# Performance work log

Hardware: AMD Instinct MI355X
Metric: run time of the kernel (lower is better)

Reference implementation:

```python
import jax, jax.numpy as jnp
import numpy as np

N_NODES = 100000
N_EDGES = 1600000
IN_CH, EDGE_DIM, HIDDEN, OUT_CH = 3, 3, 64, 1


def setup_inputs() -> dict:
    key = jax.random.key(0)
    ks = jax.random.split(key, 10)
    x = jax.random.normal(ks[0], (N_NODES, IN_CH), dtype=jnp.float32)
    edge_index = jax.random.randint(ks[1], (2, N_EDGES), 0, N_NODES, dtype=jnp.int64)
    edge_attr = jax.random.normal(ks[2], (N_EDGES, EDGE_DIM), dtype=jnp.float32)
    # Linear params (torch Linear: y = x @ W.T + b); we store W as (in, out)
    s1 = 1.0 / np.sqrt(IN_CH + EDGE_DIM)
    W1 = jax.random.uniform(ks[3], (IN_CH + EDGE_DIM, HIDDEN), jnp.float32, -s1, s1)
    b1 = jax.random.uniform(ks[4], (HIDDEN,), jnp.float32, -s1, s1)
    s2 = 1.0 / np.sqrt(HIDDEN + EDGE_DIM)
    W2 = jax.random.uniform(ks[5], (HIDDEN + EDGE_DIM, HIDDEN), jnp.float32, -s2, s2)
    b2 = jax.random.uniform(ks[6], (HIDDEN,), jnp.float32, -s2, s2)
    s3 = 1.0 / np.sqrt(HIDDEN)
    W3 = jax.random.uniform(ks[7], (HIDDEN, OUT_CH), jnp.float32, -s3, s3)
    b3 = jax.random.uniform(ks[8], (OUT_CH,), jnp.float32, -s3, s3)
    return {"x": x, "edge_index": edge_index, "edge_attr": edge_attr,
            "W1": W1, "b1": b1, "W2": W2, "b2": b2, "W3": W3, "b3": b3}


def _edge_conv(h, src, dst, edge_attr, W, b, n_nodes):
    # gather source node features, concat edge_attr, linear, scatter-add at dst
    msg = jnp.concatenate([h[src], edge_attr], axis=-1) @ W + b  # [E, out]
    return jax.ops.segment_sum(msg, dst, num_segments=n_nodes)   # [N, out]


def reference(x, edge_index, edge_attr, W1, b1, W2, b2, W3, b3):
    src, dst = edge_index[0], edge_index[1]  # PyG source_to_target: aggregate at edge_index[1]
    n = x.shape[0]
    h = jax.nn.relu(_edge_conv(x, src, dst, edge_attr, W1, b1, n))
    h = jax.nn.relu(_edge_conv(h, src, dst, edge_attr, W2, b2, n))
    return h @ W3 + b3  # (n_nodes, 1) anomaly logits
```

## Files before the change

### kernel.cpp

```cpp
#include <hip/hip_runtime.h>

#define N_NODES 100000
#define N_EDGES 1600000
#define NCHUNK 512
#define CHUNK_E (N_EDGES / NCHUNK)
#define BSHIFT 6
#define BMASK 63
#define NBUCK 1563
#define CAP 16
#define CSRB 1536
#define REC_CAP 1536


typedef unsigned int uint4_ev __attribute__((ext_vector_type(4)));
typedef short bf16x8 __attribute__((ext_vector_type(8)));
typedef float f32x4 __attribute__((ext_vector_type(4)));

__device__ __forceinline__ unsigned short f2bf(float f) {
    unsigned int u = __float_as_uint(f);
    unsigned int r = (u + 0x7fff + ((u >> 16) & 1)) >> 16;
    return (unsigned short)r;
}
__device__ __forceinline__ unsigned int pack2bf(float a, float b) {
    return (unsigned int)f2bf(a) | ((unsigned int)f2bf(b) << 16);
}
__device__ __forceinline__ float bflo(unsigned int v) { return __uint_as_float(v << 16); }
__device__ __forceinline__ float bfhi(unsigned int v) { return __uint_as_float(v & 0xffff0000u); }

__device__ __forceinline__ float4 nt_load4(const float4* p) {
    uint4_ev v = __builtin_nontemporal_load((const uint4_ev*)p);
    return make_float4(__uint_as_float(v.x), __uint_as_float(v.y),
                       __uint_as_float(v.z), __uint_as_float(v.w));
}

__device__ __forceinline__ int wave_incl_scan(int v, int lane) {
#pragma unroll
    for (int off = 1; off < 64; off <<= 1) {
        int t = __shfl_up(v, off, 64);
        if (lane >= off) v += t;
    }
    return v;
}

__global__ __launch_bounds__(1024) void k_scatter(const int* __restrict__ ei,
                                                  const float* __restrict__ ea,
                                                  const float* __restrict__ W2,
                                                  unsigned short* __restrict__ wpk,
                                                  const float* __restrict__ x,
                                                  float4* __restrict__ xp,
                                                  int* __restrict__ cnt,
                                                  float4* __restrict__ stg) {
    const int g = blockIdx.x, t = threadIdx.x;
    if (g > NCHUNK) {
        int i = (g - NCHUNK - 1) * 1024 + t;
        if (i < N_NODES)
            xp[i] = make_float4(x[i * 3 + 0], x[i * 3 + 1], x[i * 3 + 2], 0.f);
        return;
    }
    if (g == NCHUNK) {
        if (t < 512) {
            int lane = t & 63, hh = (t >> 6) & 1, nt = t >> 7;
            int col = nt * 16 + (lane & 15);
            int k0 = hh * 32 + (lane >> 4) * 8;
#pragma unroll
            for (int j = 0; j < 8; j++)
                wpk[t * 8 + j] = f2bf(W2[(k0 + j) * 64 + col]);
        }
        return;
    }
    __shared__ int cur[NBUCK];
    for (int i = t; i < NBUCK; i += 1024) cur[i] = 0;
    __syncthreads();
    const int base = g * CHUNK_E;
    for (int i = t; i < CHUNK_E; i += 1024) {
        int e = base + i;
        int src = ei[e];
        int dst = ei[N_EDGES + e];
        float a0 = ea[(size_t)e * 3 + 0];
        float a1 = ea[(size_t)e * 3 + 1];
        float a2 = ea[(size_t)e * 3 + 2];
        int b = dst >> BSHIFT;
        int p = atomicAdd(&cur[b], 1);
        if (p < CAP) {
            unsigned pk = (unsigned)src | ((unsigned)(dst & BMASK) << 17);
            stg[((size_t)g * NBUCK + b) * CAP + p] =
                make_float4(__uint_as_float(pk), a0, a1, a2);
        }
    }
    __syncthreads();
    for (int i = t; i < NBUCK; i += 1024) cnt[g * NBUCK + i] = cur[i];
}

__global__ __launch_bounds__(256) void k_finalize(
    const float4* __restrict__ stg, const int* __restrict__ cnt,
    const float4* __restrict__ xp, const float* __restrict__ W1,
    const float* __restrict__ b1, const float* __restrict__ W2,
    const float* __restrict__ b2, const bf16x8* __restrict__ wpk,
    int* __restrict__ csr, int* __restrict__ rowinfo,
    unsigned int* __restrict__ zu, unsigned int* __restrict__ eu) {
    __shared__ float4 rec[REC_CAP];
    __shared__ int sbase[513];
    __shared__ int hist[64], lofs[64], curq[64];
    __shared__ float sU[64 * 3], sT[64 * 3];
    __shared__ int ws4[4];
    const int b = blockIdx.x, t = threadIdx.x;
    const int lane = t & 63, w = t >> 6;
    int c0 = min(cnt[(size_t)(2 * t) * NBUCK + b], CAP);
    int c1 = min(cnt[(size_t)(2 * t + 1) * NBUCK + b], CAP);
    int s = c0 + c1;
    int inc = wave_incl_scan(s, lane);
    if (lane == 63) ws4[w] = inc;
    __syncthreads();
    int wo = 0;
    for (int k = 0; k < w; k++) wo += ws4[k];
    int ex = wo + inc - s;
    sbase[2 * t] = ex;
    sbase[2 * t + 1] = ex + c0;
    if (t == 255) sbase[512] = ex + s;
    if (t < 64) hist[t] = 0;
    __syncthreads();
    const int cntb = sbase[512];
    float4 r_[6];
#pragma unroll
    for (int k = 0; k < 6; k++) {
        int i = t + k * 256;
        if (i < cntb) {
            int lo = 0, hi = 512;
#pragma unroll
            for (int it = 0; it < 9; it++) {
                int mid = (lo + hi) >> 1;
                if (sbase[mid] <= i) lo = mid; else hi = mid;
            }
            r_[k] = nt_load4(&stg[((size_t)lo * NBUCK + b) * CAP + (i - sbase[lo])]);
        }
    }
#pragma unroll
    for (int k = 0; k < 6; k++) {
        int i = t + k * 256;
        if (i < cntb) atomicAdd(&hist[__float_as_uint(r_[k].x) >> 17], 1);
    }
    __syncthreads();
    if (t < 64) {
        int v = hist[t];
        int in2 = wave_incl_scan(v, t);
        lofs[t] = in2 - v;
        curq[t] = in2 - v;
    }
    __syncthreads();
#pragma unroll
    for (int k = 0; k < 6; k++) {
        int i = t + k * 256;
        if (i < cntb) {
            int p = atomicAdd(&curq[__float_as_uint(r_[k].x) >> 17], 1);
            if (p < REC_CAP) rec[p] = r_[k];
        }
    }
    __syncthreads();
    {
        const int l = t >> 2, sub = t & 3;
        const int n = b * 64 + l;
        const int d = hist[l], lo = lofs[l];
        float u0 = 0, u1 = 0, u2 = 0, t0 = 0, t1 = 0, t2 = 0;
        for (int j = sub; j < d; j += 4) {
            float4 r = rec[lo + j];
            unsigned pk = __float_as_uint(r.x);
            int src = pk & 0x1FFFF;
            csr[b * CSRB + lo + j] = src;
            t0 += r.y; t1 += r.z; t2 += r.w;
            float4 xv = xp[src];
            u0 += xv.x; u1 += xv.y; u2 += xv.z;
        }
#pragma unroll
        for (int off = 1; off <= 2; off <<= 1) {
            u0 += __shfl_xor(u0, off, 64); u1 += __shfl_xor(u1, off, 64);
            u2 += __shfl_xor(u2, off, 64); t0 += __shfl_xor(t0, off, 64);
            t1 += __shfl_xor(t1, off, 64); t2 += __shfl_xor(t2, off, 64);
        }
        if (sub == 0) {
            sU[l * 3 + 0] = u0; sU[l * 3 + 1] = u1; sU[l * 3 + 2] = u2;
            sT[l * 3 + 0] = t0; sT[l * 3 + 1] = t1; sT[l * 3 + 2] = t2;
            if (n < N_NODES)
                rowinfo[n] = (int)(((unsigned)(b * CSRB + lo) << 8) | (unsigned)d);
        }
    }
    __syncthreads();
    const int tb = b * 64 + w * 16;
    if (tb >= N_NODES) return;
    const int col = lane & 15;
    const int q = lane >> 4;
    const int ln = w * 16 + col;
    const float d = (float)hist[ln];
    const float u0 = sU[ln * 3], u1 = sU[ln * 3 + 1], u2 = sU[ln * 3 + 2];
    const float t0 = sT[ln * 3], t1 = sT[ln * 3 + 1], t2 = sT[ln * 3 + 2];
    bf16x8 af[2];
#pragma unroll
    for (int h = 0; h < 2; h++) {
#pragma unroll
        for (int j = 0; j < 8; j++) {
            int c = h * 32 + q * 8 + j;
            float a = d * b1[c];
            a = fmaf(u0, W1[0 * 64 + c], a);
            a = fmaf(u1, W1[1 * 64 + c], a);
            a = fmaf(u2, W1[2 * 64 + c], a);
            a = fmaf(t0, W1[3 * 64 + c], a);
            a = fmaf(t1, W1[4 * 64 + c], a);
            a = fmaf(t2, W1[5 * 64 + c], a);
            af[h][j] = (short)f2bf(fmaxf(a, 0.f));
        }
    }
    f32x4 acc[4];
#pragma unroll
    for (int nt = 0; nt < 4; nt++) {
        bf16x8 b0 = wpk[(nt * 2 + 0) * 64 + lane];
        bf16x8 b1f = wpk[(nt * 2 + 1) * 64 + lane];
        f32x4 a = {0.f, 0.f, 0.f, 0.f};
        a = __builtin_amdgcn_mfma_f32_16x16x32_bf16(af[0], b0, a, 0, 0, 0);
        a = __builtin_amdgcn_mfma_f32_16x16x32_bf16(af[1], b1f, a, 0, 0, 0);
        acc[nt] = a;
    }
#pragma unroll
    for (int nt = 0; nt < 4; nt++) {
#pragma unroll
        for (int r = 0; r < 4; r++) {
            float v = acc[nt][r];
            float pv = __shfl_xor(v, 1, 64);
            if ((lane & 1) == 0) {
                int nr = tb + q * 4 + r;
                zu[(size_t)nr * 32 + nt * 8 + (col >> 1)] = pack2bf(v, pv);
            }
        }
    }
    const float eb = b2[lane];
    const float w64 = W2[64 * 64 + lane];
    const float w65 = W2[65 * 64 + lane];
    const float w66 = W2[66 * 64 + lane];
#pragma unroll 4
    for (int mm = 0; mm < 16; mm++) {
        int lm = w * 16 + mm;
        float dd = (float)hist[lm];
        float s0 = sT[lm * 3], s1 = sT[lm * 3 + 1], s2 = sT[lm * 3 + 2];
        float e = dd * eb;
        e = fmaf(s0, w64, e); e = fmaf(s1, w65, e); e = fmaf(s2, w66, e);
        float pe = __shfl_xor(e, 1, 64);
        if ((lane & 1) == 0)
            eu[(size_t)(tb + mm) * 32 + (lane >> 1)] = pack2bf(e, pe);
    }
}

__global__ __launch_bounds__(256) void k_agg(
    const unsigned int* __restrict__ zu, const unsigned int* __restrict__ eu,
    const int* __restrict__ rowinfo, const int* __restrict__ csr,
    const float* __restrict__ W3, const float* __restrict__ b3,
    float* __restrict__ out) {
    const int lane = threadIdx.x & 63;
    const int li = lane & 15;
    const int q = li & 7;
    const int r = li >> 3;
    const int n = blockIdx.x * 16 + (threadIdx.x >> 4);

    float cw3[8];
#pragma unroll
    for (int m = 0; m < 8; m++) cw3[m] = W3[8 * q + m];
    const float b3v = b3[0];

    const unsigned ri = (unsigned)rowinfo[n];
    const int start = (int)(ri >> 8), end = start + (int)(ri & 255u);
    float S[8];
#pragma unroll
    for (int m = 0; m < 8; m++) S[m] = 0.f;

    for (int c = start; c < end; c += 16) {
        int idx[8];
        float mk[8];
        uint4 v[8];
#pragma unroll
        for (int u = 0; u < 8; u++) {
            int i = c + 2 * u + r;
            bool ok = i < end;
            mk[u] = ok ? 1.f : 0.f;
            idx[u] = csr[ok ? i : start];
        }
#pragma unroll
        for (int u = 0; u < 8; u++)
            v[u] = *(const uint4*)&zu[(size_t)idx[u] * 32 + q * 4];
#pragma unroll
        for (int u = 0; u < 8; u++) {
            S[0] = fmaf(mk[u], bflo(v[u].x), S[0]); S[1] = fmaf(mk[u], bfhi(v[u].x), S[1]);
            S[2] = fmaf(mk[u], bflo(v[u].y), S[2]); S[3] = fmaf(mk[u], bfhi(v[u].y), S[3]);
            S[4] = fmaf(mk[u], bflo(v[u].z), S[4]); S[5] = fmaf(mk[u], bfhi(v[u].z), S[5]);
            S[6] = fmaf(mk[u], bflo(v[u].w), S[6]); S[7] = fmaf(mk[u], bfhi(v[u].w), S[7]);
        }
    }
#pragma unroll
    for (int m = 0; m < 8; m++) S[m] += __shfl_xor(S[m], 8, 64);

    const uint4 ev = *(const uint4*)&eu[(size_t)n * 32 + q * 4];
    float contrib;
    {
        float h0 = fmaxf(S[0] + bflo(ev.x), 0.f);
        float h1v = fmaxf(S[1] + bfhi(ev.x), 0.f);
        float h2v = fmaxf(S[2] + bflo(ev.y), 0.f);
        float h3 = fmaxf(S[3] + bfhi(ev.y), 0.f);
        float h4 = fmaxf(S[4] + bflo(ev.z), 0.f);
        float h5 = fmaxf(S[5] + bfhi(ev.z), 0.f);
        float h6 = fmaxf(S[6] + bflo(ev.w), 0.f);
        float h7 = fmaxf(S[7] + bfhi(ev.w), 0.f);
        contrib = h0 * cw3[0];
        contrib = fmaf(h1v, cw3[1], contrib);
        contrib = fmaf(h2v, cw3[2], contrib);
        contrib = fmaf(h3, cw3[3], contrib);
        contrib = fmaf(h4, cw3[4], contrib);
        contrib = fmaf(h5, cw3[5], contrib);
        contrib = fmaf(h6, cw3[6], contrib);
        contrib = fmaf(h7, cw3[7], contrib);
    }
    contrib += __shfl_xor(contrib, 1, 64);
    contrib += __shfl_xor(contrib, 2, 64);
    contrib += __shfl_xor(contrib, 4, 64);
    if (li == 0) out[n] = contrib + b3v;
}

extern "C" void kernel_launch(void* const* d_in, const int* in_sizes, int n_in,
                              void* d_out, int out_size, void* d_ws, size_t ws_size,
                              hipStream_t stream) {
    const float* x  = (const float*)d_in[0];
    const int*   ei = (const int*)d_in[1];
    const float* ea = (const float*)d_in[2];
    const float* W1 = (const float*)d_in[3];
    const float* b1 = (const float*)d_in[4];
    const float* W2 = (const float*)d_in[5];
    const float* b2 = (const float*)d_in[6];
    const float* W3 = (const float*)d_in[7];
    const float* b3 = (const float*)d_in[8];
    float* out = (float*)d_out;

    char* ws = (char*)d_ws;
    int*    cnt     = (int*)(ws + 0);
    int*    rowinfo = (int*)(ws + 3201024);
    int*    csr     = (int*)(ws + 3601152);
    unsigned int* zu = (unsigned int*)(ws + 13204224);
    unsigned int* eu = (unsigned int*)(ws + 26004224);
    unsigned short* wpk = (unsigned short*)(ws + 38804224);
    float4* xp  = (float4*)(ws + 38812416);
    float4* stg = (float4*)(ws + 40412416);

    k_scatter<<<NCHUNK + 99, 1024, 0, stream>>>(ei, ea, W2, wpk, x, xp, cnt, stg);
    k_finalize<<<NBUCK, 256, 0, stream>>>(stg, cnt, xp, W1, b1, W2, b2,
                                          (const bf16x8*)wpk, csr, rowinfo, zu, eu);
    k_agg<<<N_NODES / 16, 256, 0, stream>>>(zu, eu, rowinfo, csr, W3, b3, out);
}
```

Before: 183.3 us.

## Use byte counts and one-thread-per-chunk gathering in finalize with 512 threads

```diff
diff --git a/kernel.cpp b/kernel.cpp
--- a/kernel.cpp
+++ b/kernel.cpp
@@ -9,7 +9,7 @@
 #define NBUCK 1563
 #define CAP 16
 #define CSRB 1536
-#define REC_CAP 1536
+#define REC_CAP 1280
 
 
 typedef unsigned int uint4_ev __attribute__((ext_vector_type(4)));
@@ -48,7 +48,7 @@
                                                   unsigned short* __restrict__ wpk,
                                                   const float* __restrict__ x,
                                                   float4* __restrict__ xp,
-                                                  int* __restrict__ cnt,
+                                                  unsigned char* __restrict__ cnt8,
                                                   float4* __restrict__ stg) {
     const int g = blockIdx.x, t = threadIdx.x;
     if (g > NCHUNK) {
@@ -88,80 +88,49 @@
         }
     }
     __syncthreads();
-    for (int i = t; i < NBUCK; i += 1024) cnt[g * NBUCK + i] = cur[i];
-}
-
-__global__ __launch_bounds__(256) void k_finalize(
-    const float4* __restrict__ stg, const int* __restrict__ cnt,
+    for (int i = t; i < NBUCK; i += 1024)
+        cnt8[(size_t)g * NBUCK + i] = (unsigned char)min(cur[i], 255);
+}
+
+__global__ __launch_bounds__(512) void k_finalize(
+    const float4* __restrict__ stg, const unsigned char* __restrict__ cnt8,
     const float4* __restrict__ xp, const float* __restrict__ W1,
     const float* __restrict__ b1, const float* __restrict__ W2,
     const float* __restrict__ b2, const bf16x8* __restrict__ wpk,
     int* __restrict__ csr, int* __restrict__ rowinfo,
     unsigned int* __restrict__ zu, unsigned int* __restrict__ eu) {
     __shared__ float4 rec[REC_CAP];
-    __shared__ int sbase[513];
     __shared__ int hist[64], lofs[64], curq[64];
     __shared__ float sU[64 * 3], sT[64 * 3];
-    __shared__ int ws4[4];
     const int b = blockIdx.x, t = threadIdx.x;
     const int lane = t & 63, w = t >> 6;
-    int c0 = min(cnt[(size_t)(2 * t) * NBUCK + b], CAP);
-    int c1 = min(cnt[(size_t)(2 * t + 1) * NBUCK + b], CAP);
-    int s = c0 + c1;
-    int inc = wave_incl_scan(s, lane);
-    if (lane == 63) ws4[w] = inc;
-    __syncthreads();
-    int wo = 0;
-    for (int k = 0; k < w; k++) wo += ws4[k];
-    int ex = wo + inc - s;
-    sbase[2 * t] = ex;
-    sbase[2 * t + 1] = ex + c0;
-    if (t == 255) sbase[512] = ex + s;
+    const int cc = min((int)cnt8[(size_t)t * NBUCK + b], CAP);
+    const size_t sb = ((size_t)t * NBUCK + b) * CAP;
     if (t < 64) hist[t] = 0;
     __syncthreads();
-    const int cntb = sbase[512];
-    float4 r_[6];
-#pragma unroll
-    for (int k = 0; k < 6; k++) {
-        int i = t + k * 256;
-        if (i < cntb) {
-            int lo = 0, hi = 512;
-#pragma unroll
-            for (int it = 0; it < 9; it++) {
-                int mid = (lo + hi) >> 1;
-                if (sbase[mid] <= i) lo = mid; else hi = mid;
-            }
-            r_[k] = nt_load4(&stg[((size_t)lo * NBUCK + b) * CAP + (i - sbase[lo])]);
-        }
-    }
-#pragma unroll
-    for (int k = 0; k < 6; k++) {
-        int i = t + k * 256;
-        if (i < cntb) atomicAdd(&hist[__float_as_uint(r_[k].x) >> 17], 1);
-    }
+    const float* stgf = (const float*)stg;
+    for (int j = 0; j < cc; ++j)
+        atomicAdd(&hist[__float_as_uint(stgf[(sb + j) * 4]) >> 17], 1);
     __syncthreads();
     if (t < 64) {
         int v = hist[t];
-        int in2 = wave_incl_scan(v, t);
-        lofs[t] = in2 - v;
-        curq[t] = in2 - v;
-    }
-    __syncthreads();
-#pragma unroll
-    for (int k = 0; k < 6; k++) {
-        int i = t + k * 256;
-        if (i < cntb) {
-            int p = atomicAdd(&curq[__float_as_uint(r_[k].x) >> 17], 1);
-            if (p < REC_CAP) rec[p] = r_[k];
-        }
+        int inc = wave_incl_scan(v, t);
+        lofs[t] = inc - v;
+        curq[t] = inc - v;
+    }
+    __syncthreads();
+    for (int j = 0; j < cc; ++j) {
+        float4 r = nt_load4(&stg[sb + j]);
+        int p = atomicAdd(&curq[__float_as_uint(r.x) >> 17], 1);
+        if (p < REC_CAP) rec[p] = r;
     }
     __syncthreads();
     {
-        const int l = t >> 2, sub = t & 3;
+        const int l = t >> 3, sub = t & 7;
         const int n = b * 64 + l;
         const int d = hist[l], lo = lofs[l];
         float u0 = 0, u1 = 0, u2 = 0, t0 = 0, t1 = 0, t2 = 0;
-        for (int j = sub; j < d; j += 4) {
+        for (int j = sub; j < d; j += 8) {
             float4 r = rec[lo + j];
             unsigned pk = __float_as_uint(r.x);
             int src = pk & 0x1FFFF;
@@ -171,7 +140,7 @@
             u0 += xv.x; u1 += xv.y; u2 += xv.z;
         }
 #pragma unroll
-        for (int off = 1; off <= 2; off <<= 1) {
+        for (int off = 1; off <= 4; off <<= 1) {
             u0 += __shfl_xor(u0, off, 64); u1 += __shfl_xor(u1, off, 64);
             u2 += __shfl_xor(u2, off, 64); t0 += __shfl_xor(t0, off, 64);
             t1 += __shfl_xor(t1, off, 64); t2 += __shfl_xor(t2, off, 64);
@@ -184,6 +153,7 @@
         }
     }
     __syncthreads();
+    if (w >= 4) return;
     const int tb = b * 64 + w * 16;
     if (tb >= N_NODES) return;
     const int col = lane & 15;
@@ -335,17 +305,17 @@
     float* out = (float*)d_out;
 
     char* ws = (char*)d_ws;
-    int*    cnt     = (int*)(ws + 0);
-    int*    rowinfo = (int*)(ws + 3201024);
-    int*    csr     = (int*)(ws + 3601152);
-    unsigned int* zu = (unsigned int*)(ws + 13204224);
-    unsigned int* eu = (unsigned int*)(ws + 26004224);
-    unsigned short* wpk = (unsigned short*)(ws + 38804224);
-    float4* xp  = (float4*)(ws + 38812416);
-    float4* stg = (float4*)(ws + 40412416);
-
-    k_scatter<<<NCHUNK + 99, 1024, 0, stream>>>(ei, ea, W2, wpk, x, xp, cnt, stg);
-    k_finalize<<<NBUCK, 256, 0, stream>>>(stg, cnt, xp, W1, b1, W2, b2,
+    unsigned char* cnt8 = (unsigned char*)(ws + 0);
+    int*    rowinfo = (int*)(ws + 800256);
+    int*    csr     = (int*)(ws + 1200384);
+    unsigned int* zu = (unsigned int*)(ws + 10803456);
+    unsigned int* eu = (unsigned int*)(ws + 23603456);
+    unsigned short* wpk = (unsigned short*)(ws + 36403456);
+    float4* xp  = (float4*)(ws + 36411648);
+    float4* stg = (float4*)(ws + 38011648);
+
+    k_scatter<<<NCHUNK + 99, 1024, 0, stream>>>(ei, ea, W2, wpk, x, xp, cnt8, stg);
+    k_finalize<<<NBUCK, 512, 0, stream>>>(stg, cnt8, xp, W1, b1, W2, b2,
                                           (const bf16x8*)wpk, csr, rowinfo, zu, eu);
     k_agg<<<N_NODES / 16, 256, 0, stream>>>(zu, eu, rowinfo, csr, W3, b3, out);
 }
```

Result: slower. 202.5 us (+10.4%).
